# Performance work log

Hardware: AMD Instinct MI355X
Metric: run time of the kernel (lower is better)

The kernel has to match this reference:

```python
import jax, jax.numpy as jnp
import numpy as np

S, I, H, O = 4096, 64, 1024, 1


def setup_inputs() -> dict:
    key = jax.random.key(0)
    ks = jax.random.split(key, 8)
    k = 1.0 / np.sqrt(H)  # torch LSTM/Linear init scale
    u = lambda kk, shp: jax.random.uniform(kk, shp, jnp.float32, -k, k)
    return {
        "input_seq": jax.random.normal(ks[0], (S, I), jnp.float32),
        "W_ih": u(ks[1], (4 * H, I)),
        "W_hh": u(ks[2], (4 * H, H)),
        "b_ih": u(ks[3], (4 * H,)),
        "b_hh": u(ks[4], (4 * H,)),
        "W_lin": u(ks[5], (O, H)),
        "b_lin": u(ks[6], (O,)),
    }


def reference(input_seq, W_ih, W_hh, b_ih, b_hh, W_lin, b_lin):
    # Precompute input contributions to all gates in one GEMM: [S, 4H]
    x_gates = input_seq @ W_ih.T + (b_ih + b_hh)

    def step(carry, xg):
        h, c = carry
        g = xg + h @ W_hh.T  # [4H], gate order i, f, g, o (torch convention)
        i, f, gg, o = jnp.split(g, 4)
        i = jax.nn.sigmoid(i)
        f = jax.nn.sigmoid(f)
        gg = jnp.tanh(gg)
        o = jax.nn.sigmoid(o)
        c = f * c + i * gg
        h = o * jnp.tanh(c)
        return (h, c), None

    h0 = jnp.zeros((H,), x_gates.dtype)
    c0 = jnp.zeros((H,), x_gates.dtype)
    (h_last, _), _ = jax.lax.scan(step, (h0, c0), x_gates)
    # original applies linear to every step then takes [-1]; equivalent to
    # projecting only the last hidden state
    return h_last @ W_lin.T + b_lin  # [O]
```

## Files before the change

kernel.cpp:

```cpp
#include <hip/hip_runtime.h>


#define SEQ_LEN 4096
#define HID 1024
#define NBLK 128
#define TPB 512
#define HPB 8

__device__ __forceinline__ float fast_sigmoid(float x) {
    return __builtin_amdgcn_rcpf(1.0f + __builtin_amdgcn_exp2f(-1.4426950408889634f * x));
}
__device__ __forceinline__ float fast_tanh(float x) {
    return fmaf(-2.0f, __builtin_amdgcn_rcpf(1.0f + __builtin_amdgcn_exp2f(2.8853900817779268f * x)), 1.0f);
}

__global__ void lstm_init_kernel(unsigned long long* ws) {
    int t = threadIdx.x;
    #pragma unroll
    for (int k = 0; k < 8; ++k) ws[t + 256 * k] = 0ull;
}

__global__ __launch_bounds__(TPB, 1) void lstm_persistent_kernel(
    const float* __restrict__ input,
    const float* __restrict__ W_ih,
    const float* __restrict__ W_hh,
    const float* __restrict__ b_ih,
    const float* __restrict__ b_hh,
    const float* __restrict__ W_lin,
    const float* __restrict__ b_lin,
    float* __restrict__ out,
    unsigned long long* __restrict__ ws)
{
    const int t   = threadIdx.x;
    const int b   = blockIdx.x;
    const int w   = t >> 6;
    const int l   = t & 63;
    const int grp = l >> 4;
    const int sl  = l & 15;
    const int j   = HPB * b + w;
    const int row = grp * HID + j;

    unsigned long long* slot0 = ws;
    unsigned long long* slot1 = ws + HID;

    __shared__ float4 wlds4[17 * TPB];
    __shared__ float  hs[2][HID];
    __shared__ unsigned long long pub[HPB];
    __shared__ float  red[HPB];

    {
        const float4* Whh4 = (const float4*)(W_hh + (size_t)row * HID);
        #pragma unroll
        for (int c = 0; c < 16; ++c)
            wlds4[c * TPB + t] = Whh4[sl + 16 * c];
        wlds4[16 * TPB + t] = ((const float4*)(W_ih + (size_t)row * 64))[sl];
    }
    float bias[4];
    #pragma unroll
    for (int q = 0; q < 4; ++q) bias[q] = b_ih[q * HID + j] + b_hh[q * HID + j];
    if (t < HPB) pub[t] = 0ull;
    __syncthreads();

    const float4 W0  = wlds4[ 0 * TPB + t];
    const float4 W1  = wlds4[ 1 * TPB + t];
    const float4 W2  = wlds4[ 2 * TPB + t];
    const float4 W3  = wlds4[ 3 * TPB + t];
    const float4 W4  = wlds4[ 4 * TPB + t];
    const float4 W5  = wlds4[ 5 * TPB + t];
    const float4 W6  = wlds4[ 6 * TPB + t];
    const float4 W7  = wlds4[ 7 * TPB + t];
    const float4 W8  = wlds4[ 8 * TPB + t];
    const float4 W9  = wlds4[ 9 * TPB + t];
    const float4 W10 = wlds4[10 * TPB + t];
    const float4 W11 = wlds4[11 * TPB + t];
    const float4 W12 = wlds4[12 * TPB + t];
    const float4 W13 = wlds4[13 * TPB + t];
    const float4 W14 = wlds4[14 * TPB + t];
    const float4 W15 = wlds4[15 * TPB + t];
    const float4 W16 = wlds4[16 * TPB + t];

    const float4* xin4 = (const float4*)input;
    float c_state = 0.0f;

    for (int s = 0; s < SEQ_LEN; ++s) {
        float4 x4 = xin4[s * 16 + sl];

        unsigned long long* rs = (s & 1) ? slot1 : slot0;
        const unsigned tag = (unsigned)s;
        unsigned long long v0, v1;
        bool r0 = false, r1 = false;
        do {
            if (!r0) { v0 = __hip_atomic_load(&rs[t      ], __ATOMIC_RELAXED, __HIP_MEMORY_SCOPE_AGENT);
                       r0 = ((unsigned)(v0 >> 32) == tag); }
            if (!r1) { v1 = __hip_atomic_load(&rs[t + 512], __ATOMIC_RELAXED, __HIP_MEMORY_SCOPE_AGENT);
                       r1 = ((unsigned)(v1 >> 32) == tag); }
        } while (!(r0 && r1));

        float* hsb = hs[s & 1];
        hsb[t      ] = __uint_as_float((unsigned)(v0 & 0xffffffffull));
        hsb[t + 512] = __uint_as_float((unsigned)(v1 & 0xffffffffull));

        __syncthreads();

        const float4* hs4 = (const float4*)hsb;
        float a0 = 0.f, a1 = 0.f, a2 = 0.f, a3 = 0.f;
        #define FMA_CHUNK(Wc, c, acc) { float4 h4_ = hs4[16 * (c) + sl];      \
            acc = fmaf((Wc).x, h4_.x, acc); acc = fmaf((Wc).y, h4_.y, acc);   \
            acc = fmaf((Wc).z, h4_.z, acc); acc = fmaf((Wc).w, h4_.w, acc); }
        FMA_CHUNK(W0,  0, a0) FMA_CHUNK(W1,  1, a1)
        FMA_CHUNK(W2,  2, a2) FMA_CHUNK(W3,  3, a3)
        FMA_CHUNK(W4,  4, a0) FMA_CHUNK(W5,  5, a1)
        FMA_CHUNK(W6,  6, a2) FMA_CHUNK(W7,  7, a3)
        FMA_CHUNK(W8,  8, a0) FMA_CHUNK(W9,  9, a1)
        FMA_CHUNK(W10, 10, a2) FMA_CHUNK(W11, 11, a3)
        FMA_CHUNK(W12, 12, a0) FMA_CHUNK(W13, 13, a1)
        FMA_CHUNK(W14, 14, a2) FMA_CHUNK(W15, 15, a3)
        #undef FMA_CHUNK
        a0 = fmaf(W16.x, x4.x, a0); a1 = fmaf(W16.y, x4.y, a1);
        a2 = fmaf(W16.z, x4.z, a2); a3 = fmaf(W16.w, x4.w, a3);
        float acc = (a0 + a1) + (a2 + a3);

        acc += __shfl_xor(acc, 1);
        acc += __shfl_xor(acc, 2);
        acc += __shfl_xor(acc, 4);
        acc += __shfl_xor(acc, 8);

        float gi = __shfl(acc, 0)  + bias[0];
        float gf = __shfl(acc, 16) + bias[1];
        float gg = __shfl(acc, 32) + bias[2];
        float go = __shfl(acc, 48) + bias[3];

        float ig = fast_sigmoid(gi);
        float fg = fast_sigmoid(gf);
        float cg = fast_tanh(gg);
        float og = fast_sigmoid(go);
        c_state  = fmaf(fg, c_state, ig * cg);
        float hn = og * fast_tanh(c_state);

        const unsigned ntag = (unsigned)(s + 1);
        if (l == 0) {
            unsigned long long pv = ((unsigned long long)ntag << 32) |
                                    (unsigned long long)__float_as_uint(hn);
            __hip_atomic_store(&pub[w], pv, __ATOMIC_RELAXED, __HIP_MEMORY_SCOPE_WORKGROUP);
        }
        if (w == 0 && l < HPB) {
            unsigned long long pv;
            do {
                pv = __hip_atomic_load(&pub[l], __ATOMIC_RELAXED, __HIP_MEMORY_SCOPE_WORKGROUP);
            } while ((unsigned)(pv >> 32) != ntag);
            unsigned long long* wsl = (s & 1) ? slot0 : slot1;
            __hip_atomic_store(&wsl[HPB * b + l], pv, __ATOMIC_RELAXED, __HIP_MEMORY_SCOPE_AGENT);
        }
    }

    if (b == 0) {
        const unsigned tag = (unsigned)SEQ_LEN;
        unsigned long long v0, v1;
        bool r0 = false, r1 = false;
        do {
            if (!r0) { v0 = __hip_atomic_load(&slot0[t      ], __ATOMIC_RELAXED, __HIP_MEMORY_SCOPE_AGENT);
                       r0 = ((unsigned)(v0 >> 32) == tag); }
            if (!r1) { v1 = __hip_atomic_load(&slot0[t + 512], __ATOMIC_RELAXED, __HIP_MEMORY_SCOPE_AGENT);
                       r1 = ((unsigned)(v1 >> 32) == tag); }
        } while (!(r0 && r1));
        float p = __uint_as_float((unsigned)(v0 & 0xffffffffull)) * W_lin[t] +
                  __uint_as_float((unsigned)(v1 & 0xffffffffull)) * W_lin[t + 512];
        #pragma unroll
        for (int m = 32; m >= 1; m >>= 1) p += __shfl_xor(p, m);
        if (l == 0) red[w] = p;
        __syncthreads();
        if (t == 0) {
            float r = 0.f;
            #pragma unroll
            for (int k = 0; k < HPB; ++k) r += red[k];
            out[0] = r + b_lin[0];
        }
    }
}

extern "C" void kernel_launch(void* const* d_in, const int* in_sizes, int n_in,
                              void* d_out, int out_size, void* d_ws, size_t ws_size,
                              hipStream_t stream) {
    const float* input = (const float*)d_in[0];
    const float* W_ih  = (const float*)d_in[1];
    const float* W_hh  = (const float*)d_in[2];
    const float* b_ih  = (const float*)d_in[3];
    const float* b_hh  = (const float*)d_in[4];
    const float* W_lin = (const float*)d_in[5];
    const float* b_lin = (const float*)d_in[6];
    float* out = (float*)d_out;
    unsigned long long* ws = (unsigned long long*)d_ws;

    hipLaunchKernelGGL(lstm_init_kernel, dim3(1), dim3(256), 0, stream, ws);

    void* args[] = { (void*)&input, (void*)&W_ih, (void*)&W_hh, (void*)&b_ih,
                     (void*)&b_hh, (void*)&W_lin, (void*)&b_lin, (void*)&out, (void*)&ws };
    (void)hipLaunchCooperativeKernel((void*)lstm_persistent_kernel, dim3(NBLK), dim3(TPB),
                                     args, 0, stream);
}
```

Before: 8.294 ms.

## Halve persistent block count with 1024-thread blocks, 16 hidden units each

Changes the persistent LSTM grid from 128 blocks of 512 threads to 64 blocks of 1024 threads, so each block owns 16 hidden units. Weights are staged into registers in two passes through a half-size shared buffer. Only the first half of each block polls the global h slots. The aim is to cut the number of blocks taking part in the per-step cross-block handoff and the number of global polling readers. The cost is longer intra-block barriers and half as many CUs doing the matvec, with more work per CU each step.

Result: slower. 8.693 ms (+4.8%).

```diff
diff --git a/kernel.cpp b/kernel.cpp
--- a/kernel.cpp
+++ b/kernel.cpp
@@ -3,9 +3,9 @@
 
 #define SEQ_LEN 4096
 #define HID 1024
-#define NBLK 128
-#define TPB 512
-#define HPB 8
+#define NBLK 64
+#define TPB 1024
+#define HPB 16
 
 __device__ __forceinline__ float fast_sigmoid(float x) {
     return __builtin_amdgcn_rcpf(1.0f + __builtin_amdgcn_exp2f(-1.4426950408889634f * x));
@@ -39,70 +39,73 @@
     const int sl  = l & 15;
     const int j   = HPB * b + w;
     const int row = grp * HID + j;
+    const int th  = t & 511;
+    const int half = t >> 9;
 
     unsigned long long* slot0 = ws;
     unsigned long long* slot1 = ws + HID;
 
-    __shared__ float4 wlds4[17 * TPB];
+    __shared__ float4 wstage[17 * 512];
     __shared__ float  hs[2][HID];
     __shared__ unsigned long long pub[HPB];
     __shared__ float  red[HPB];
 
-    {
-        const float4* Whh4 = (const float4*)(W_hh + (size_t)row * HID);
-        #pragma unroll
-        for (int c = 0; c < 16; ++c)
-            wlds4[c * TPB + t] = Whh4[sl + 16 * c];
-        wlds4[16 * TPB + t] = ((const float4*)(W_ih + (size_t)row * 64))[sl];
+    float4 W0, W1, W2, W3, W4, W5, W6, W7, W8, W9, W10, W11, W12, W13, W14, W15, W16;
+    const float4* Whh4 = (const float4*)(W_hh + (size_t)row * HID);
+    #pragma unroll
+    for (int pass = 0; pass < 2; ++pass) {
+        if (half == pass) {
+            #pragma unroll
+            for (int c = 0; c < 16; ++c)
+                wstage[c * 512 + th] = Whh4[sl + 16 * c];
+            wstage[16 * 512 + th] = ((const float4*)(W_ih + (size_t)row * 64))[sl];
+        }
+        __syncthreads();
+        if (half == pass) {
+            W0  = wstage[ 0 * 512 + th];  W1  = wstage[ 1 * 512 + th];
+            W2  = wstage[ 2 * 512 + th];  W3  = wstage[ 3 * 512 + th];
+            W4  = wstage[ 4 * 512 + th];  W5  = wstage[ 5 * 512 + th];
+            W6  = wstage[ 6 * 512 + th];  W7  = wstage[ 7 * 512 + th];
+            W8  = wstage[ 8 * 512 + th];  W9  = wstage[ 9 * 512 + th];
+            W10 = wstage[10 * 512 + th];  W11 = wstage[11 * 512 + th];
+            W12 = wstage[12 * 512 + th];  W13 = wstage[13 * 512 + th];
+            W14 = wstage[14 * 512 + th];  W15 = wstage[15 * 512 + th];
+            W16 = wstage[16 * 512 + th];
+        }
+        __syncthreads();
     }
+
     float bias[4];
     #pragma unroll
     for (int q = 0; q < 4; ++q) bias[q] = b_ih[q * HID + j] + b_hh[q * HID + j];
     if (t < HPB) pub[t] = 0ull;
-    __syncthreads();
-
-    const float4 W0  = wlds4[ 0 * TPB + t];
-    const float4 W1  = wlds4[ 1 * TPB + t];
-    const float4 W2  = wlds4[ 2 * TPB + t];
-    const float4 W3  = wlds4[ 3 * TPB + t];
-    const float4 W4  = wlds4[ 4 * TPB + t];
-    const float4 W5  = wlds4[ 5 * TPB + t];
-    const float4 W6  = wlds4[ 6 * TPB + t];
-    const float4 W7  = wlds4[ 7 * TPB + t];
-    const float4 W8  = wlds4[ 8 * TPB + t];
-    const float4 W9  = wlds4[ 9 * TPB + t];
-    const float4 W10 = wlds4[10 * TPB + t];
-    const float4 W11 = wlds4[11 * TPB + t];
-    const float4 W12 = wlds4[12 * TPB + t];
-    const float4 W13 = wlds4[13 * TPB + t];
-    const float4 W14 = wlds4[14 * TPB + t];
-    const float4 W15 = wlds4[15 * TPB + t];
-    const float4 W16 = wlds4[16 * TPB + t];
 
     const float4* xin4 = (const float4*)input;
     float c_state = 0.0f;
+    __syncthreads();
 
     for (int s = 0; s < SEQ_LEN; ++s) {
         float4 x4 = xin4[s * 16 + sl];
 
-        unsigned long long* rs = (s & 1) ? slot1 : slot0;
-        const unsigned tag = (unsigned)s;
-        unsigned long long v0, v1;
-        bool r0 = false, r1 = false;
-        do {
-            if (!r0) { v0 = __hip_atomic_load(&rs[t      ], __ATOMIC_RELAXED, __HIP_MEMORY_SCOPE_AGENT);
-                       r0 = ((unsigned)(v0 >> 32) == tag); }
-            if (!r1) { v1 = __hip_atomic_load(&rs[t + 512], __ATOMIC_RELAXED, __HIP_MEMORY_SCOPE_AGENT);
-                       r1 = ((unsigned)(v1 >> 32) == tag); }
-        } while (!(r0 && r1));
-
-        float* hsb = hs[s & 1];
-        hsb[t      ] = __uint_as_float((unsigned)(v0 & 0xffffffffull));
-        hsb[t + 512] = __uint_as_float((unsigned)(v1 & 0xffffffffull));
-
-        __syncthreads();
-
-        const float4* hs4 = (const float4*)hsb;
+        if (half == 0) {
+            unsigned long long* rs = (s & 1) ? slot1 : slot0;
+            const unsigned tag = (unsigned)s;
+            unsigned long long v0, v1;
+            bool r0 = false, r1 = false;
+            do {
+                if (!r0) { v0 = __hip_atomic_load(&rs[th      ], __ATOMIC_RELAXED, __HIP_MEMORY_SCOPE_AGENT);
+                           r0 = ((unsigned)(v0 >> 32) == tag); }
+                if (!r1) { v1 = __hip_atomic_load(&rs[th + 512], __ATOMIC_RELAXED, __HIP_MEMORY_SCOPE_AGENT);
+                           r1 = ((unsigned)(v1 >> 32) == tag); }
+            } while (!(r0 && r1));
+            float* hsb = hs[s & 1];
+            hsb[th      ] = __uint_as_float((unsigned)(v0 & 0xffffffffull));
+            hsb[th + 512] = __uint_as_float((unsigned)(v1 & 0xffffffffull));
+        }
+
+        __syncthreads();
+
+        const float4* hs4 = (const float4*)hs[s & 1];
         float a0 = 0.f, a1 = 0.f, a2 = 0.f, a3 = 0.f;
         #define FMA_CHUNK(Wc, c, acc) { float4 h4_ = hs4[16 * (c) + sl];      \
             acc = fmaf((Wc).x, h4_.x, acc); acc = fmaf((Wc).y, h4_.y, acc);   \
@@ -154,17 +157,20 @@
     }
 
     if (b == 0) {
-        const unsigned tag = (unsigned)SEQ_LEN;
-        unsigned long long v0, v1;
-        bool r0 = false, r1 = false;
-        do {
-            if (!r0) { v0 = __hip_atomic_load(&slot0[t      ], __ATOMIC_RELAXED, __HIP_MEMORY_SCOPE_AGENT);
-                       r0 = ((unsigned)(v0 >> 32) == tag); }
-            if (!r1) { v1 = __hip_atomic_load(&slot0[t + 512], __ATOMIC_RELAXED, __HIP_MEMORY_SCOPE_AGENT);
-                       r1 = ((unsigned)(v1 >> 32) == tag); }
-        } while (!(r0 && r1));
-        float p = __uint_as_float((unsigned)(v0 & 0xffffffffull)) * W_lin[t] +
-                  __uint_as_float((unsigned)(v1 & 0xffffffffull)) * W_lin[t + 512];
+        float p = 0.0f;
+        if (half == 0) {
+            const unsigned tag = (unsigned)SEQ_LEN;
+            unsigned long long v0, v1;
+            bool r0 = false, r1 = false;
+            do {
+                if (!r0) { v0 = __hip_atomic_load(&slot0[th      ], __ATOMIC_RELAXED, __HIP_MEMORY_SCOPE_AGENT);
+                           r0 = ((unsigned)(v0 >> 32) == tag); }
+                if (!r1) { v1 = __hip_atomic_load(&slot0[th + 512], __ATOMIC_RELAXED, __HIP_MEMORY_SCOPE_AGENT);
+                           r1 = ((unsigned)(v1 >> 32) == tag); }
+            } while (!(r0 && r1));
+            p = __uint_as_float((unsigned)(v0 & 0xffffffffull)) * W_lin[th] +
+                __uint_as_float((unsigned)(v1 & 0xffffffffull)) * W_lin[th + 512];
+        }
         #pragma unroll
         for (int m = 32; m >= 1; m >>= 1) p += __shfl_xor(p, m);
         if (l == 0) red[w] = p;
```

## Replace per-element tagged h polling with global arrival counter barrier

Applied to the files above, without the earlier changes.

Each step previously polled all 1024 tagged 64-bit hidden-state slots until every tag matched. Now each block writes plain float h values, waits for its stores with vmcnt(0), then bumps one global counter. A single thread spins on that counter before the block reads h as packed 64-bit loads. This cuts per-step polling traffic and halves the h payload, but every step now depends on one contended atomic plus an extra __syncthreads. Relaxed atomics with no release/acquire fence also risk visibility ordering issues.

Measured after the change: 13.90 ms. +67.6%, slower.

```diff
diff --git a/kernel.cpp b/kernel.cpp
--- a/kernel.cpp
+++ b/kernel.cpp
@@ -14,10 +14,11 @@
     return fmaf(-2.0f, __builtin_amdgcn_rcpf(1.0f + __builtin_amdgcn_exp2f(2.8853900817779268f * x)), 1.0f);
 }
 
-__global__ void lstm_init_kernel(unsigned long long* ws) {
+__global__ void lstm_init_kernel(float* ws) {
     int t = threadIdx.x;
     #pragma unroll
-    for (int k = 0; k < 8; ++k) ws[t + 256 * k] = 0ull;
+    for (int k = 0; k < 8; ++k) ws[t + 256 * k] = 0.0f;
+    if (t == 0) *((unsigned*)(ws + 2 * HID)) = 0u;
 }
 
 __global__ __launch_bounds__(TPB, 1) void lstm_persistent_kernel(
@@ -29,7 +30,7 @@
     const float* __restrict__ W_lin,
     const float* __restrict__ b_lin,
     float* __restrict__ out,
-    unsigned long long* __restrict__ ws)
+    float* __restrict__ ws)
 {
     const int t   = threadIdx.x;
     const int b   = blockIdx.x;
@@ -40,8 +41,9 @@
     const int j   = HPB * b + w;
     const int row = grp * HID + j;
 
-    unsigned long long* slot0 = ws;
-    unsigned long long* slot1 = ws + HID;
+    float* hslot0 = ws;
+    float* hslot1 = ws + HID;
+    unsigned* counter = (unsigned*)(ws + 2 * HID);
 
     __shared__ float4 wlds4[17 * TPB];
     __shared__ float  hs[2][HID];
@@ -85,24 +87,26 @@
     for (int s = 0; s < SEQ_LEN; ++s) {
         float4 x4 = xin4[s * 16 + sl];
 
-        unsigned long long* rs = (s & 1) ? slot1 : slot0;
-        const unsigned tag = (unsigned)s;
-        unsigned long long v0, v1;
-        bool r0 = false, r1 = false;
-        do {
-            if (!r0) { v0 = __hip_atomic_load(&rs[t      ], __ATOMIC_RELAXED, __HIP_MEMORY_SCOPE_AGENT);
-                       r0 = ((unsigned)(v0 >> 32) == tag); }
-            if (!r1) { v1 = __hip_atomic_load(&rs[t + 512], __ATOMIC_RELAXED, __HIP_MEMORY_SCOPE_AGENT);
-                       r1 = ((unsigned)(v1 >> 32) == tag); }
-        } while (!(r0 && r1));
-
-        float* hsb = hs[s & 1];
-        hsb[t      ] = __uint_as_float((unsigned)(v0 & 0xffffffffull));
-        hsb[t + 512] = __uint_as_float((unsigned)(v1 & 0xffffffffull));
-
-        __syncthreads();
-
-        const float4* hs4 = (const float4*)hsb;
+        if (t == 0) {
+            const unsigned tgt = (unsigned)s * (unsigned)NBLK;
+            while (__hip_atomic_load(counter, __ATOMIC_RELAXED,
+                                     __HIP_MEMORY_SCOPE_AGENT) < tgt) {}
+        }
+        __syncthreads();
+
+        {
+            const float* rsl = (s & 1) ? hslot1 : hslot0;
+            unsigned long long hv = __hip_atomic_load(
+                (unsigned long long*)rsl + t, __ATOMIC_RELAXED,
+                __HIP_MEMORY_SCOPE_AGENT);
+            float2 hp;
+            hp.x = __uint_as_float((unsigned)(hv & 0xffffffffull));
+            hp.y = __uint_as_float((unsigned)(hv >> 32));
+            ((float2*)hs[s & 1])[t] = hp;
+        }
+        __syncthreads();
+
+        const float4* hs4 = (const float4*)hs[s & 1];
         float a0 = 0.f, a1 = 0.f, a2 = 0.f, a3 = 0.f;
         #define FMA_CHUNK(Wc, c, acc) { float4 h4_ = hs4[16 * (c) + sl];      \
             acc = fmaf((Wc).x, h4_.x, acc); acc = fmaf((Wc).y, h4_.y, acc);   \
@@ -143,28 +147,36 @@
                                     (unsigned long long)__float_as_uint(hn);
             __hip_atomic_store(&pub[w], pv, __ATOMIC_RELAXED, __HIP_MEMORY_SCOPE_WORKGROUP);
         }
-        if (w == 0 && l < HPB) {
-            unsigned long long pv;
-            do {
-                pv = __hip_atomic_load(&pub[l], __ATOMIC_RELAXED, __HIP_MEMORY_SCOPE_WORKGROUP);
-            } while ((unsigned)(pv >> 32) != ntag);
-            unsigned long long* wsl = (s & 1) ? slot0 : slot1;
-            __hip_atomic_store(&wsl[HPB * b + l], pv, __ATOMIC_RELAXED, __HIP_MEMORY_SCOPE_AGENT);
+        if (w == 0) {
+            if (l < HPB) {
+                unsigned long long pv;
+                do {
+                    pv = __hip_atomic_load(&pub[l], __ATOMIC_RELAXED, __HIP_MEMORY_SCOPE_WORKGROUP);
+                } while ((unsigned)(pv >> 32) != ntag);
+                float* wsl = (s & 1) ? hslot0 : hslot1;
+                __hip_atomic_store(&wsl[HPB * b + l],
+                                   __uint_as_float((unsigned)(pv & 0xffffffffull)),
+                                   __ATOMIC_RELAXED, __HIP_MEMORY_SCOPE_AGENT);
+            }
+            asm volatile("s_waitcnt vmcnt(0)" ::: "memory");
+            if (l == 0)
+                __hip_atomic_fetch_add(counter, 1u, __ATOMIC_RELAXED,
+                                       __HIP_MEMORY_SCOPE_AGENT);
         }
     }
 
     if (b == 0) {
-        const unsigned tag = (unsigned)SEQ_LEN;
-        unsigned long long v0, v1;
-        bool r0 = false, r1 = false;
-        do {
-            if (!r0) { v0 = __hip_atomic_load(&slot0[t      ], __ATOMIC_RELAXED, __HIP_MEMORY_SCOPE_AGENT);
-                       r0 = ((unsigned)(v0 >> 32) == tag); }
-            if (!r1) { v1 = __hip_atomic_load(&slot0[t + 512], __ATOMIC_RELAXED, __HIP_MEMORY_SCOPE_AGENT);
-                       r1 = ((unsigned)(v1 >> 32) == tag); }
-        } while (!(r0 && r1));
-        float p = __uint_as_float((unsigned)(v0 & 0xffffffffull)) * W_lin[t] +
-                  __uint_as_float((unsigned)(v1 & 0xffffffffull)) * W_lin[t + 512];
+        if (t == 0) {
+            const unsigned tgt = (unsigned)SEQ_LEN * (unsigned)NBLK;
+            while (__hip_atomic_load(counter, __ATOMIC_RELAXED,
+                                     __HIP_MEMORY_SCOPE_AGENT) < tgt) {}
+        }
+        __syncthreads();
+        unsigned long long hv = __hip_atomic_load(
+            (unsigned long long*)hslot0 + t, __ATOMIC_RELAXED,
+            __HIP_MEMORY_SCOPE_AGENT);
+        float p = __uint_as_float((unsigned)(hv & 0xffffffffull)) * W_lin[2 * t] +
+                  __uint_as_float((unsigned)(hv >> 32))          * W_lin[2 * t + 1];
         #pragma unroll
         for (int m = 32; m >= 1; m >>= 1) p += __shfl_xor(p, m);
         if (l == 0) red[w] = p;
@@ -189,7 +201,7 @@
     const float* W_lin = (const float*)d_in[5];
     const float* b_lin = (const float*)d_in[6];
     float* out = (float*)d_out;
-    unsigned long long* ws = (unsigned long long*)d_ws;
+    float* ws  = (float*)d_ws;
 
     hipLaunchKernelGGL(lstm_init_kernel, dim3(1), dim3(256), 0, stream, ws);
 
```
